# Kernel tuning notes

Measured on AMD Instinct MI355X. Metric: run time of the kernel, lower is better.

The kernel has to match this reference:

```python
import jax, jax.numpy as jnp
import numpy as np

B, T, E, H = 4, 2048, 4096, 128

def setup_inputs() -> dict:
    key = jax.random.key(0)
    ks = jax.random.split(key, 5)
    x = jax.random.normal(ks[0], (B, T, E), dtype=jnp.float32)
    pos_emb = jax.random.normal(ks[1], (B, T, E), dtype=jnp.float32)
    # torch nn.Linear(E, H, bias=False) weights have shape [H, E]
    scale = 1.0 / np.sqrt(E)
    Wq = jax.random.normal(ks[2], (H, E), dtype=jnp.float32) * scale
    Wk = jax.random.normal(ks[3], (H, E), dtype=jnp.float32) * scale
    Wv = jax.random.normal(ks[4], (H, E), dtype=jnp.float32) * scale
    return {"x": x, "pos_emb": pos_emb, "Wq": Wq, "Wk": Wk, "Wv": Wv}

def reference(x, pos_emb, Wq, Wk, Wv):
    Bd, Td, Ed = x.shape
    q = jnp.einsum('bte,he->bth', x, Wq)        # [B,T,H]
    k = jnp.einsum('bte,he->bth', pos_emb, Wk)  # [B,T,H] (key is computed from pos_emb, per source)
    v = jnp.einsum('bte,he->bth', x, Wv)        # [B,T,H]
    # NOTE: source scales by full model dim E**-0.5, not head_size**-0.5
    scores = jnp.einsum('bqh,bkh->bqk', q, k) * (Ed ** -0.5)  # [B,T,T]
    causal = jnp.tril(jnp.ones((Td, Td), dtype=bool))
    scores = jnp.where(causal[None, :, :], scores, -jnp.inf)
    attn = jax.nn.softmax(scores, axis=-1)
    out = jnp.einsum('bqk,bkh->bqh', attn, v)   # [B,T,H]
    return out
```

## Files before the change

### kernel.cpp

```cpp
#include <hip/hip_runtime.h>

#define BB 4
#define TT 2048
#define EE 4096
#define HH 128
#define MM (BB*TT)
#define SCALE 0.015625f

typedef short short8 __attribute__((ext_vector_type(8)));
typedef float f32x4 __attribute__((ext_vector_type(4)));
typedef unsigned short ushort_t;

__device__ __forceinline__ unsigned short f2bf(float x) {
    unsigned int u = __float_as_uint(x);
    u = (u + 0x7fffu + ((u >> 16) & 1u)) >> 16;
    return (unsigned short)u;
}

__global__ __launch_bounds__(256) void wconv(
    const float* __restrict__ Wq, const float* __restrict__ Wk,
    const float* __restrict__ Wv, ushort_t* __restrict__ Wb)
{
    const int gid = blockIdx.x * 256 + threadIdx.x;
    const int which = gid >> 16;
    const int rem = gid & 65535;
    const float* W = (which == 0) ? Wq : (which == 1) ? Wk : Wv;
    const float sc = (which == 0) ? SCALE : 1.0f;
    const float4 f0 = *(const float4*)(W + (size_t)rem * 8);
    const float4 f1 = *(const float4*)(W + (size_t)rem * 8 + 4);
    short8 pk;
    pk[0] = (short)f2bf(f0.x * sc); pk[1] = (short)f2bf(f0.y * sc);
    pk[2] = (short)f2bf(f0.z * sc); pk[3] = (short)f2bf(f0.w * sc);
    pk[4] = (short)f2bf(f1.x * sc); pk[5] = (short)f2bf(f1.y * sc);
    pk[6] = (short)f2bf(f1.z * sc); pk[7] = (short)f2bf(f1.w * sc);
    *(short8*)(Wb + (size_t)which * 524288 + (size_t)rem * 8) = pk;
}

#define ASTR 72

__global__ __launch_bounds__(256) void proj_mfma(
    const float* __restrict__ x, const float* __restrict__ pe,
    const ushort_t* __restrict__ Wb,
    ushort_t* __restrict__ qo, ushort_t* __restrict__ ko_,
    ushort_t* __restrict__ vto)
{
    const int widx = blockIdx.y >> 1;
    const int half = blockIdx.y & 1;
    const float* in = (widx == 1) ? pe : x;
    const ushort_t* W = Wb + (size_t)widx * 524288 + (size_t)half * 64 * EE;

    const int rb   = blockIdx.x * 32;
    const int tid  = threadIdx.x;
    const int lane = tid & 63, wave = tid >> 6;
    const int wr   = wave & 1, wc = wave >> 1;

    __shared__ __align__(16) ushort_t As[32 * ASTR];
    __shared__ __align__(16) ushort_t Bs[64 * ASTR];

    f32x4 acc[2];
    acc[0] = (f32x4){0.f,0.f,0.f,0.f};
    acc[1] = (f32x4){0.f,0.f,0.f,0.f};

    const int fr = lane & 15, quad = lane >> 4, ko = quad * 8;

    const int arow = tid >> 3, aoff = (tid & 7) * 8;
    const float* aptr = in + (size_t)(rb + arow) * EE + aoff;
    const int wrow0 = tid >> 3,        woff0 = (tid & 7) * 8;
    const int wrow1 = wrow0 + 32,      woff1 = woff0;

    float4 pa0 = *(const float4*)(aptr);
    float4 pa1 = *(const float4*)(aptr + 4);
    short8 pw0 = *(const short8*)(W + (size_t)wrow0 * EE + woff0);
    short8 pw1 = *(const short8*)(W + (size_t)wrow1 * EE + woff1);

    for (int k0 = 0; k0 < EE; k0 += 64) {
        {
            short8 a;
            a[0] = (short)f2bf(pa0.x); a[1] = (short)f2bf(pa0.y);
            a[2] = (short)f2bf(pa0.z); a[3] = (short)f2bf(pa0.w);
            a[4] = (short)f2bf(pa1.x); a[5] = (short)f2bf(pa1.y);
            a[6] = (short)f2bf(pa1.z); a[7] = (short)f2bf(pa1.w);
            *(short8*)&As[arow * ASTR + aoff] = a;
            *(short8*)&Bs[wrow0 * ASTR + woff0] = pw0;
            *(short8*)&Bs[wrow1 * ASTR + woff1] = pw1;
        }
        __syncthreads();

        if (k0 + 64 < EE) {
            pa0 = *(const float4*)(aptr + k0 + 64);
            pa1 = *(const float4*)(aptr + k0 + 68);
            pw0 = *(const short8*)(W + (size_t)wrow0 * EE + k0 + 64 + woff0);
            pw1 = *(const short8*)(W + (size_t)wrow1 * EE + k0 + 64 + woff1);
        }

        #pragma unroll
        for (int kk = 0; kk < 64; kk += 32) {
            const short8 af = *(short8*)&As[(wr * 16 + fr) * ASTR + kk + ko];
            #pragma unroll
            for (int t = 0; t < 2; t++) {
                const short8 bf_ = *(short8*)&Bs[(wc * 32 + t * 16 + fr) * ASTR + kk + ko];
                acc[t] = __builtin_amdgcn_mfma_f32_16x16x32_bf16(af, bf_, acc[t], 0, 0, 0);
            }
        }
        __syncthreads();
    }

    const int crow = quad * 4;
    if (widx < 2) {
        ushort_t* out = (widx == 0) ? qo : ko_;
        #pragma unroll
        for (int t = 0; t < 2; t++)
            #pragma unroll
            for (int r = 0; r < 4; r++)
                out[(size_t)(rb + wr * 16 + crow + r) * HH
                    + half * 64 + wc * 32 + t * 16 + fr] = f2bf(acc[t][r]);
    } else {
        ushort_t* T = Bs;
        #pragma unroll
        for (int t = 0; t < 2; t++)
            #pragma unroll
            for (int r = 0; r < 4; r++)
                T[(wc * 32 + t * 16 + fr) * 40 + wr * 16 + crow + r] = f2bf(acc[t][r]);
        __syncthreads();
        const int h64 = tid >> 2, m0 = (tid & 3) * 8;
        const short8 val = *(short8*)&T[h64 * 40 + m0];
        *(short8*)(vto + (size_t)(half * 64 + h64) * MM + rb + m0) = val;
    }
}

__global__ __launch_bounds__(256) void attn_mfma(
    const ushort_t* __restrict__ qb, const ushort_t* __restrict__ kbf,
    const ushort_t* __restrict__ vtb,
    float* __restrict__ OP, float* __restrict__ LP)
{
    const int b = blockIdx.z;
    const int s = blockIdx.y;
    const int t = 63 - (int)blockIdx.x;
    const int tid  = threadIdx.x;
    const int lane = tid & 63, wave = tid >> 6;
    const int fr = lane & 15, quad = lane >> 4, ko = quad * 8;

    const int q0 = t * 32;
    const int C  = (t + 2) >> 1;
    const int cs = (C + 1) >> 1;
    const int c0 = s ? cs : 0;
    const int c1 = s ? C  : cs;

    __shared__ __align__(16) ushort_t Qs[32 * 136];
    __shared__ __align__(16) ushort_t Ks[64 * 136];
    __shared__ __align__(16) ushort_t Vt[128 * 72];
    __shared__ __align__(16) ushort_t Ps[32 * 72];
    __shared__ float lred[2][32];

    for (int f = tid; f < 512; f += 256) {
        const int row = f >> 4, sg = f & 15;
        *(short8*)&Qs[row * 136 + sg * 8] =
            *(const short8*)(qb + (size_t)(b * TT + q0 + row) * HH + sg * 8);
    }

    const int rhS = (wave & 1) * 16, cqS = (wave >> 1) * 32;
    const int rhO = (wave & 1) * 16, chO = (wave >> 1) * 64;

    f32x4 oacc[4];
    #pragma unroll
    for (int i = 0; i < 4; i++) oacc[i] = (f32x4){0.f,0.f,0.f,0.f};
    float lacc[4] = {0.f, 0.f, 0.f, 0.f};

    for (int c = c0; c < c1; c++) {
        const int kb_ = c * 64;
        for (int f = tid; f < 1024; f += 256) {
            const int row = f >> 4, sg = f & 15;
            *(short8*)&Ks[row * 136 + sg * 8] =
                *(const short8*)(kbf + (size_t)(b * TT + kb_ + row) * HH + sg * 8);
        }
        for (int f = tid; f < 1024; f += 256) {
            const int h = f >> 3, sg = f & 7;
            *(short8*)&Vt[h * 72 + sg * 8] =
                *(const short8*)(vtb + (size_t)h * MM + b * TT + kb_ + sg * 8);
        }
        __syncthreads();

        f32x4 sacc[2];
        sacc[0] = (f32x4){0.f,0.f,0.f,0.f};
        sacc[1] = (f32x4){0.f,0.f,0.f,0.f};
        #pragma unroll
        for (int kk = 0; kk < 128; kk += 32) {
            const short8 af = *(short8*)&Qs[(rhS + fr) * 136 + kk + ko];
            const short8 b0 = *(short8*)&Ks[(cqS + fr) * 136 + kk + ko];
            const short8 b1 = *(short8*)&Ks[(cqS + 16 + fr) * 136 + kk + ko];
            sacc[0] = __builtin_amdgcn_mfma_f32_16x16x32_bf16(af, b0, sacc[0], 0, 0, 0);
            sacc[1] = __builtin_amdgcn_mfma_f32_16x16x32_bf16(af, b1, sacc[1], 0, 0, 0);
        }

        #pragma unroll
        for (int tl = 0; tl < 2; tl++)
            #pragma unroll
            for (int r = 0; r < 4; r++) {
                const int row = rhS + quad * 4 + r;
                const int col = cqS + tl * 16 + fr;
                const float p = ((kb_ + col) <= (q0 + row)) ? __expf(sacc[tl][r]) : 0.f;
                lacc[r] += p;
                Ps[row * 72 + col] = f2bf(p);
            }
        __syncthreads();

        #pragma unroll
        for (int ks = 0; ks < 64; ks += 32) {
            const short8 af = *(short8*)&Ps[(rhO + fr) * 72 + ks + ko];
            #pragma unroll
            for (int tl = 0; tl < 4; tl++) {
                const short8 bf_ = *(short8*)&Vt[(chO + tl * 16 + fr) * 72 + ks + ko];
                oacc[tl] = __builtin_amdgcn_mfma_f32_16x16x32_bf16(af, bf_, oacc[tl], 0, 0, 0);
            }
        }
        __syncthreads();
    }

    #pragma unroll
    for (int r = 0; r < 4; r++) {
        float v = lacc[r];
        #pragma unroll
        for (int m = 1; m < 16; m <<= 1) v += __shfl_xor(v, m);
        lacc[r] = v;
    }
    if (fr == 0) {
        #pragma unroll
        for (int r = 0; r < 4; r++)
            lred[wave >> 1][rhS + quad * 4 + r] = lacc[r];
    }
    __syncthreads();
    const int pbase = ((b * 64 + t) * 2 + s);
    if (tid < 32) LP[(size_t)pbase * 32 + tid] = lred[0][tid] + lred[1][tid];

    #pragma unroll
    for (int tl = 0; tl < 4; tl++)
        #pragma unroll
        for (int r = 0; r < 4; r++) {
            const int row = rhO + quad * 4 + r;
            const int col = chO + tl * 16 + fr;
            OP[(size_t)pbase * 4096 + row * 128 + col] = oacc[tl][r];
        }
}

__global__ __launch_bounds__(256) void combine(
    const float* __restrict__ OP, const float* __restrict__ LP,
    float* __restrict__ out)
{
    const int gid = blockIdx.x * 256 + threadIdx.x;
    const int b = gid >> 16;
    const int rem = gid & 65535;
    const int qrow = rem >> 5, h4 = rem & 31;
    const int t = qrow >> 5, r = qrow & 31;
    const int base = (b * 64 + t) * 2;
    const float l = LP[(size_t)base * 32 + r] + LP[(size_t)(base + 1) * 32 + r];
    const float inv = 1.f / l;
    const float4 a = ((const float4*)OP)[(size_t)base * 1024 + r * 32 + h4];
    const float4 c = ((const float4*)OP)[(size_t)(base + 1) * 1024 + r * 32 + h4];
    float4 res;
    res.x = (a.x + c.x) * inv; res.y = (a.y + c.y) * inv;
    res.z = (a.z + c.z) * inv; res.w = (a.w + c.w) * inv;
    ((float4*)out)[gid] = res;
}

extern "C" void kernel_launch(void* const* d_in, const int* in_sizes, int n_in,
                              void* d_out, int out_size, void* d_ws, size_t ws_size,
                              hipStream_t stream) {
    const float* x  = (const float*)d_in[0];
    const float* pe = (const float*)d_in[1];
    const float* Wq = (const float*)d_in[2];
    const float* Wk = (const float*)d_in[3];
    const float* Wv = (const float*)d_in[4];
    float* out = (float*)d_out;

    ushort_t* qb  = (ushort_t*)d_ws;
    ushort_t* kbf = qb  + (size_t)MM * HH;
    ushort_t* vtb = kbf + (size_t)MM * HH;
    ushort_t* Wb  = vtb + (size_t)MM * HH;
    float* OP = (float*)(Wb + (size_t)3 * 128 * 4096);
    float* LP = OP + (size_t)512 * 4096;

    wconv    <<<768, 256, 0, stream>>>(Wq, Wk, Wv, Wb);
    proj_mfma<<<dim3(256, 6), 256, 0, stream>>>(x, pe, Wb, qb, kbf, vtb);
    attn_mfma<<<dim3(64, 2, BB), 256, 0, stream>>>(qb, kbf, vtb, OP, LP);
    combine  <<<1024, 256, 0, stream>>>(OP, LP, out);
}
```

Baseline: 396.0 us.

## Widen projection tile to full head dim with register-resident weight fragments and double buffering

The projection kernel now computes all 128 output columns per block instead of splitting into two halves, so each fp32 input row tile is read and converted to bf16 once rather than twice. Weight fragments are loaded straight from global memory into registers instead of being staged through shared memory. The A tile is double-buffered in LDS with a 128-wide k step, which needs one barrier per step instead of two. In exchange there are half as many blocks (768), more register pressure from 16 prefetched weight fragments and four accumulators, and the non-coalesced per-lane weight loads rely on cache hits.

```diff
diff --git a/kernel.cpp b/kernel.cpp
--- a/kernel.cpp
+++ b/kernel.cpp
@@ -36,7 +36,44 @@
     *(short8*)(Wb + (size_t)which * 524288 + (size_t)rem * 8) = pk;
 }
 
-#define ASTR 72
+#define PSTR 136
+
+#define PACK8(S0, S1, A0, A1, A2, A3) \
+    S0[0]=(short)f2bf(A0.x); S0[1]=(short)f2bf(A0.y); S0[2]=(short)f2bf(A0.z); S0[3]=(short)f2bf(A0.w); \
+    S0[4]=(short)f2bf(A1.x); S0[5]=(short)f2bf(A1.y); S0[6]=(short)f2bf(A1.z); S0[7]=(short)f2bf(A1.w); \
+    S1[0]=(short)f2bf(A2.x); S1[1]=(short)f2bf(A2.y); S1[2]=(short)f2bf(A2.z); S1[3]=(short)f2bf(A2.w); \
+    S1[4]=(short)f2bf(A3.x); S1[5]=(short)f2bf(A3.y); S1[6]=(short)f2bf(A3.z); S1[7]=(short)f2bf(A3.w);
+
+#define PROJ_STEP(KB, BUF, PBC, PBN) do { \
+    const bool more_ = (KB) + 128 < EE; \
+    float4 na0, na1, na2, na3; \
+    if (more_) { \
+        const float* ap_ = aptr + (KB) + 128; \
+        na0 = *(const float4*)ap_;        na1 = *(const float4*)(ap_ + 4); \
+        na2 = *(const float4*)(ap_ + 8);  na3 = *(const float4*)(ap_ + 12); \
+        _Pragma("unroll") \
+        for (int kk = 0; kk < 4; kk++) { \
+            PBN[kk]     = *(const short8*)(wp0 + (KB) + 128 + kk * 32); \
+            PBN[4 + kk] = *(const short8*)(wp1 + (KB) + 128 + kk * 32); \
+        } \
+    } \
+    _Pragma("unroll") \
+    for (int kk = 0; kk < 4; kk++) { \
+        const short8 a0_ = *(const short8*)&As[BUF][fr * PSTR + kk * 32 + ko]; \
+        const short8 a1_ = *(const short8*)&As[BUF][(16 + fr) * PSTR + kk * 32 + ko]; \
+        acc[0][0] = __builtin_amdgcn_mfma_f32_16x16x32_bf16(a0_, PBC[kk],     acc[0][0], 0, 0, 0); \
+        acc[0][1] = __builtin_amdgcn_mfma_f32_16x16x32_bf16(a0_, PBC[4 + kk], acc[0][1], 0, 0, 0); \
+        acc[1][0] = __builtin_amdgcn_mfma_f32_16x16x32_bf16(a1_, PBC[kk],     acc[1][0], 0, 0, 0); \
+        acc[1][1] = __builtin_amdgcn_mfma_f32_16x16x32_bf16(a1_, PBC[4 + kk], acc[1][1], 0, 0, 0); \
+    } \
+    if (more_) { \
+        short8 s0_, s1_; \
+        PACK8(s0_, s1_, na0, na1, na2, na3) \
+        *(short8*)&As[(BUF) ^ 1][arow * PSTR + acol]     = s0_; \
+        *(short8*)&As[(BUF) ^ 1][arow * PSTR + acol + 8] = s1_; \
+        __syncthreads(); \
+    } \
+} while (0)
 
 __global__ __launch_bounds__(256) void proj_mfma(
     const float* __restrict__ x, const float* __restrict__ pe,
@@ -44,87 +81,81 @@
     ushort_t* __restrict__ qo, ushort_t* __restrict__ ko_,
     ushort_t* __restrict__ vto)
 {
-    const int widx = blockIdx.y >> 1;
-    const int half = blockIdx.y & 1;
+    const int widx = blockIdx.y;
     const float* in = (widx == 1) ? pe : x;
-    const ushort_t* W = Wb + (size_t)widx * 524288 + (size_t)half * 64 * EE;
+    const ushort_t* W = Wb + (size_t)widx * 524288;
 
     const int rb   = blockIdx.x * 32;
     const int tid  = threadIdx.x;
     const int lane = tid & 63, wave = tid >> 6;
-    const int wr   = wave & 1, wc = wave >> 1;
-
-    __shared__ __align__(16) ushort_t As[32 * ASTR];
-    __shared__ __align__(16) ushort_t Bs[64 * ASTR];
-
-    f32x4 acc[2];
-    acc[0] = (f32x4){0.f,0.f,0.f,0.f};
-    acc[1] = (f32x4){0.f,0.f,0.f,0.f};
-
     const int fr = lane & 15, quad = lane >> 4, ko = quad * 8;
 
-    const int arow = tid >> 3, aoff = (tid & 7) * 8;
-    const float* aptr = in + (size_t)(rb + arow) * EE + aoff;
-    const int wrow0 = tid >> 3,        woff0 = (tid & 7) * 8;
-    const int wrow1 = wrow0 + 32,      woff1 = woff0;
-
-    float4 pa0 = *(const float4*)(aptr);
-    float4 pa1 = *(const float4*)(aptr + 4);
-    short8 pw0 = *(const short8*)(W + (size_t)wrow0 * EE + woff0);
-    short8 pw1 = *(const short8*)(W + (size_t)wrow1 * EE + woff1);
-
-    for (int k0 = 0; k0 < EE; k0 += 64) {
-        {
-            short8 a;
-            a[0] = (short)f2bf(pa0.x); a[1] = (short)f2bf(pa0.y);
-            a[2] = (short)f2bf(pa0.z); a[3] = (short)f2bf(pa0.w);
-            a[4] = (short)f2bf(pa1.x); a[5] = (short)f2bf(pa1.y);
-            a[6] = (short)f2bf(pa1.z); a[7] = (short)f2bf(pa1.w);
-            *(short8*)&As[arow * ASTR + aoff] = a;
-            *(short8*)&Bs[wrow0 * ASTR + woff0] = pw0;
-            *(short8*)&Bs[wrow1 * ASTR + woff1] = pw1;
-        }
-        __syncthreads();
-
-        if (k0 + 64 < EE) {
-            pa0 = *(const float4*)(aptr + k0 + 64);
-            pa1 = *(const float4*)(aptr + k0 + 68);
-            pw0 = *(const short8*)(W + (size_t)wrow0 * EE + k0 + 64 + woff0);
-            pw1 = *(const short8*)(W + (size_t)wrow1 * EE + k0 + 64 + woff1);
-        }
-
-        #pragma unroll
-        for (int kk = 0; kk < 64; kk += 32) {
-            const short8 af = *(short8*)&As[(wr * 16 + fr) * ASTR + kk + ko];
-            #pragma unroll
-            for (int t = 0; t < 2; t++) {
-                const short8 bf_ = *(short8*)&Bs[(wc * 32 + t * 16 + fr) * ASTR + kk + ko];
-                acc[t] = __builtin_amdgcn_mfma_f32_16x16x32_bf16(af, bf_, acc[t], 0, 0, 0);
-            }
-        }
-        __syncthreads();
+    __shared__ __align__(16) ushort_t As[2][32 * PSTR];
+
+    f32x4 acc[2][2];
+    acc[0][0] = (f32x4){0.f,0.f,0.f,0.f};
+    acc[0][1] = (f32x4){0.f,0.f,0.f,0.f};
+    acc[1][0] = (f32x4){0.f,0.f,0.f,0.f};
+    acc[1][1] = (f32x4){0.f,0.f,0.f,0.f};
+
+    const int arow = tid >> 3, acol = (tid & 7) * 16;
+    const float* aptr = in + (size_t)(rb + arow) * EE + acol;
+
+    const ushort_t* wp0 = W + (size_t)(wave * 32 + fr) * EE + ko;
+    const ushort_t* wp1 = W + (size_t)(wave * 32 + 16 + fr) * EE + ko;
+
+    short8 pbA[8], pbB[8];
+
+    {
+        float4 a0 = *(const float4*)(aptr);
+        float4 a1 = *(const float4*)(aptr + 4);
+        float4 a2 = *(const float4*)(aptr + 8);
+        float4 a3 = *(const float4*)(aptr + 12);
+        #pragma unroll
+        for (int kk = 0; kk < 4; kk++) {
+            pbA[kk]     = *(const short8*)(wp0 + kk * 32);
+            pbA[4 + kk] = *(const short8*)(wp1 + kk * 32);
+        }
+        short8 s0, s1;
+        PACK8(s0, s1, a0, a1, a2, a3)
+        *(short8*)&As[0][arow * PSTR + acol]     = s0;
+        *(short8*)&As[0][arow * PSTR + acol + 8] = s1;
+        __syncthreads();
+    }
+
+    for (int k0 = 0; k0 < EE; k0 += 256) {
+        PROJ_STEP(k0,       0, pbA, pbB);
+        PROJ_STEP(k0 + 128, 1, pbB, pbA);
     }
 
     const int crow = quad * 4;
     if (widx < 2) {
         ushort_t* out = (widx == 0) ? qo : ko_;
         #pragma unroll
-        for (int t = 0; t < 2; t++)
+        for (int rg = 0; rg < 2; rg++)
             #pragma unroll
-            for (int r = 0; r < 4; r++)
-                out[(size_t)(rb + wr * 16 + crow + r) * HH
-                    + half * 64 + wc * 32 + t * 16 + fr] = f2bf(acc[t][r]);
+            for (int cg = 0; cg < 2; cg++)
+                #pragma unroll
+                for (int r = 0; r < 4; r++)
+                    out[(size_t)(rb + rg * 16 + crow + r) * HH
+                        + wave * 32 + cg * 16 + fr] = f2bf(acc[rg][cg][r]);
     } else {
-        ushort_t* T = Bs;
-        #pragma unroll
-        for (int t = 0; t < 2; t++)
+        __syncthreads();
+        ushort_t* T = (ushort_t*)As;
+        #pragma unroll
+        for (int rg = 0; rg < 2; rg++)
             #pragma unroll
-            for (int r = 0; r < 4; r++)
-                T[(wc * 32 + t * 16 + fr) * 40 + wr * 16 + crow + r] = f2bf(acc[t][r]);
-        __syncthreads();
-        const int h64 = tid >> 2, m0 = (tid & 3) * 8;
-        const short8 val = *(short8*)&T[h64 * 40 + m0];
-        *(short8*)(vto + (size_t)(half * 64 + h64) * MM + rb + m0) = val;
+            for (int cg = 0; cg < 2; cg++)
+                #pragma unroll
+                for (int r = 0; r < 4; r++)
+                    T[(wave * 32 + cg * 16 + fr) * 40 + rg * 16 + crow + r]
+                        = f2bf(acc[rg][cg][r]);
+        __syncthreads();
+        const int col = tid >> 1, m0 = (tid & 1) * 16;
+        const short8 v0 = *(short8*)&T[col * 40 + m0];
+        const short8 v1 = *(short8*)&T[col * 40 + m0 + 8];
+        *(short8*)(vto + (size_t)col * MM + rb + m0)     = v0;
+        *(short8*)(vto + (size_t)col * MM + rb + m0 + 8) = v1;
     }
 }
 
@@ -280,7 +311,7 @@
     float* LP = OP + (size_t)512 * 4096;
 
     wconv    <<<768, 256, 0, stream>>>(Wq, Wk, Wv, Wb);
-    proj_mfma<<<dim3(256, 6), 256, 0, stream>>>(x, pe, Wb, qb, kbf, vtb);
+    proj_mfma<<<dim3(256, 3), 256, 0, stream>>>(x, pe, Wb, qb, kbf, vtb);
     attn_mfma<<<dim3(64, 2, BB), 256, 0, stream>>>(qb, kbf, vtb, OP, LP);
     combine  <<<1024, 256, 0, stream>>>(OP, LP, out);
 }
```

Result: faster. 386.6 us (-2.4%).

## Retile projection GEMM to 128x128 tiles with split-K and async LDS loads

Applied to the files above, without the earlier changes.

The projection GEMM now gives each block a 128-row tile covering all 128 head columns, with a 4x4 MFMA accumulator per wave. Each block handles a quarter of the K dimension, and a new combine kernel sums the fp32 partials and writes bf16 q/k and transposed v. Weight tiles are staged into double-buffered LDS with global_load_lds, and the fp32 input is prefetched in registers. The intent is to stop re-reading x twice per weight half and to raise MFMA reuse. In exchange there is an extra kernel and fp32 partial traffic through a workspace that is shared with the attention partial buffers.

```diff
diff --git a/kernel.cpp b/kernel.cpp
--- a/kernel.cpp
+++ b/kernel.cpp
@@ -10,11 +10,18 @@
 typedef short short8 __attribute__((ext_vector_type(8)));
 typedef float f32x4 __attribute__((ext_vector_type(4)));
 typedef unsigned short ushort_t;
+typedef unsigned int u32;
 
 __device__ __forceinline__ unsigned short f2bf(float x) {
     unsigned int u = __float_as_uint(x);
     u = (u + 0x7fffu + ((u >> 16) & 1u)) >> 16;
     return (unsigned short)u;
+}
+
+__device__ __forceinline__ void gl_lds16(const ushort_t* g, ushort_t* l) {
+    __builtin_amdgcn_global_load_lds(
+        (const __attribute__((address_space(1))) u32*)(g),
+        (__attribute__((address_space(3))) u32*)(l), 16, 0, 0);
 }
 
 __global__ __launch_bounds__(256) void wconv(
@@ -36,95 +43,175 @@
     *(short8*)(Wb + (size_t)which * 524288 + (size_t)rem * 8) = pk;
 }
 
-#define ASTR 72
+#define KSPLIT 4
+#define KSPAN  1024
+#define KSTEP  64
+#define NSTEPS 16
+#define ASTRIDE 72
 
 __global__ __launch_bounds__(256) void proj_mfma(
     const float* __restrict__ x, const float* __restrict__ pe,
-    const ushort_t* __restrict__ Wb,
+    const ushort_t* __restrict__ Wb, float* __restrict__ Pp)
+{
+    const int mb   = blockIdx.x;
+    const int widx = blockIdx.y;
+    const int sp   = blockIdx.z;
+    const float* in = (widx == 1) ? pe : x;
+    const ushort_t* W = Wb + (size_t)widx * (128 * EE);
+
+    const int rb    = mb * 128;
+    const int kbase = sp * KSPAN;
+
+    const int tid  = threadIdx.x;
+    const int lane = tid & 63, wave = tid >> 6;
+    const int wr = wave & 1, wc = wave >> 1;
+    const int fr = lane & 15, quad = lane >> 4, ko = quad * 8;
+
+    __shared__ __align__(16) ushort_t Asl[128 * ASTRIDE];
+    __shared__ __align__(16) ushort_t Bsl[2][128 * KSTEP];
+
+    f32x4 acc[4][4];
+    #pragma unroll
+    for (int m = 0; m < 4; m++)
+        #pragma unroll
+        for (int n = 0; n < 4; n++) acc[m][n] = (f32x4){0.f,0.f,0.f,0.f};
+
+    const int arow = tid >> 1;
+    const int acol = (tid & 1) * 32;
+    const float* aptr = in + (size_t)(rb + arow) * EE + kbase + acol;
+
+    const ushort_t* bsrc = W + (size_t)(tid >> 3) * EE + kbase + (tid & 7) * 8;
+    const int bdst = tid * 8;
+
+    float4 ar[8];
+
+#define LOAD_A(KOFS) do { \
+    const float* p_ = aptr + (KOFS); \
+    _Pragma("unroll") \
+    for (int j = 0; j < 8; j++) ar[j] = *(const float4*)(p_ + j * 4); \
+} while (0)
+
+#define STAGE_B(KOFS, BUF) do { \
+    _Pragma("unroll") \
+    for (int j = 0; j < 4; j++) \
+        gl_lds16(bsrc + (KOFS) + (size_t)j * 32 * EE, \
+                 &Bsl[BUF][bdst + j * 2048]); \
+} while (0)
+
+#define WRITE_A() do { \
+    _Pragma("unroll") \
+    for (int j = 0; j < 4; j++) { \
+        short8 s_; \
+        const float4 a0_ = ar[2*j], a1_ = ar[2*j+1]; \
+        s_[0]=(short)f2bf(a0_.x); s_[1]=(short)f2bf(a0_.y); \
+        s_[2]=(short)f2bf(a0_.z); s_[3]=(short)f2bf(a0_.w); \
+        s_[4]=(short)f2bf(a1_.x); s_[5]=(short)f2bf(a1_.y); \
+        s_[6]=(short)f2bf(a1_.z); s_[7]=(short)f2bf(a1_.w); \
+        *(short8*)&Asl[arow * ASTRIDE + acol + j * 8] = s_; \
+    } \
+} while (0)
+
+    LOAD_A(0);
+    STAGE_B(0, 0);
+    WRITE_A();
+    __syncthreads();
+
+    for (int s = 0; s < NSTEPS; s++) {
+        const int buf = s & 1;
+        const bool more = (s + 1 < NSTEPS);
+        if (more) {
+            LOAD_A((s + 1) * KSTEP);
+            STAGE_B((s + 1) * KSTEP, buf ^ 1);
+        }
+        #pragma unroll
+        for (int h = 0; h < 2; h++) {
+            short8 af[4], bf_[4];
+            #pragma unroll
+            for (int m = 0; m < 4; m++)
+                af[m] = *(short8*)&Asl[(wr*64 + m*16 + fr) * ASTRIDE + h*32 + ko];
+            #pragma unroll
+            for (int n = 0; n < 4; n++)
+                bf_[n] = *(short8*)&Bsl[buf][(wc*64 + n*16 + fr) * KSTEP + h*32 + ko];
+            #pragma unroll
+            for (int m = 0; m < 4; m++)
+                #pragma unroll
+                for (int n = 0; n < 4; n++)
+                    acc[m][n] = __builtin_amdgcn_mfma_f32_16x16x32_bf16(
+                        af[m], bf_[n], acc[m][n], 0, 0, 0);
+        }
+        __syncthreads();
+        if (more) {
+            WRITE_A();
+            __syncthreads();
+        }
+    }
+
+    float* P = Pp + ((size_t)(widx * KSPLIT + sp) * MM + rb) * HH;
+    #pragma unroll
+    for (int m = 0; m < 4; m++)
+        #pragma unroll
+        for (int n = 0; n < 4; n++)
+            #pragma unroll
+            for (int r = 0; r < 4; r++)
+                P[(size_t)(wr*64 + m*16 + quad*4 + r) * HH
+                  + wc*64 + n*16 + fr] = acc[m][n][r];
+
+#undef LOAD_A
+#undef STAGE_B
+#undef WRITE_A
+}
+
+__global__ __launch_bounds__(256) void projcomb(
+    const float* __restrict__ Pp,
     ushort_t* __restrict__ qo, ushort_t* __restrict__ ko_,
     ushort_t* __restrict__ vto)
 {
-    const int widx = blockIdx.y >> 1;
-    const int half = blockIdx.y & 1;
-    const float* in = (widx == 1) ? pe : x;
-    const ushort_t* W = Wb + (size_t)widx * 524288 + (size_t)half * 64 * EE;
-
-    const int rb   = blockIdx.x * 32;
+    const int mb   = blockIdx.x;
+    const int widx = blockIdx.y;
     const int tid  = threadIdx.x;
-    const int lane = tid & 63, wave = tid >> 6;
-    const int wr   = wave & 1, wc = wave >> 1;
-
-    __shared__ __align__(16) ushort_t As[32 * ASTR];
-    __shared__ __align__(16) ushort_t Bs[64 * ASTR];
-
-    f32x4 acc[2];
-    acc[0] = (f32x4){0.f,0.f,0.f,0.f};
-    acc[1] = (f32x4){0.f,0.f,0.f,0.f};
-
-    const int fr = lane & 15, quad = lane >> 4, ko = quad * 8;
-
-    const int arow = tid >> 3, aoff = (tid & 7) * 8;
-    const float* aptr = in + (size_t)(rb + arow) * EE + aoff;
-    const int wrow0 = tid >> 3,        woff0 = (tid & 7) * 8;
-    const int wrow1 = wrow0 + 32,      woff1 = woff0;
-
-    float4 pa0 = *(const float4*)(aptr);
-    float4 pa1 = *(const float4*)(aptr + 4);
-    short8 pw0 = *(const short8*)(W + (size_t)wrow0 * EE + woff0);
-    short8 pw1 = *(const short8*)(W + (size_t)wrow1 * EE + woff1);
-
-    for (int k0 = 0; k0 < EE; k0 += 64) {
-        {
-            short8 a;
-            a[0] = (short)f2bf(pa0.x); a[1] = (short)f2bf(pa0.y);
-            a[2] = (short)f2bf(pa0.z); a[3] = (short)f2bf(pa0.w);
-            a[4] = (short)f2bf(pa1.x); a[5] = (short)f2bf(pa1.y);
-            a[6] = (short)f2bf(pa1.z); a[7] = (short)f2bf(pa1.w);
-            *(short8*)&As[arow * ASTR + aoff] = a;
-            *(short8*)&Bs[wrow0 * ASTR + woff0] = pw0;
-            *(short8*)&Bs[wrow1 * ASTR + woff1] = pw1;
-        }
-        __syncthreads();
-
-        if (k0 + 64 < EE) {
-            pa0 = *(const float4*)(aptr + k0 + 64);
-            pa1 = *(const float4*)(aptr + k0 + 68);
-            pw0 = *(const short8*)(W + (size_t)wrow0 * EE + k0 + 64 + woff0);
-            pw1 = *(const short8*)(W + (size_t)wrow1 * EE + k0 + 64 + woff1);
-        }
-
-        #pragma unroll
-        for (int kk = 0; kk < 64; kk += 32) {
-            const short8 af = *(short8*)&As[(wr * 16 + fr) * ASTR + kk + ko];
-            #pragma unroll
-            for (int t = 0; t < 2; t++) {
-                const short8 bf_ = *(short8*)&Bs[(wc * 32 + t * 16 + fr) * ASTR + kk + ko];
-                acc[t] = __builtin_amdgcn_mfma_f32_16x16x32_bf16(af, bf_, acc[t], 0, 0, 0);
-            }
-        }
-        __syncthreads();
-    }
-
-    const int crow = quad * 4;
+    const int m0 = mb * 64;
+    const int r_ = tid >> 2;
+    const int h0 = (tid & 3) * 32;
+
+    __shared__ ushort_t T[128 * 72];
+
+    const float* base = Pp + ((size_t)widx * KSPLIT * MM + m0 + r_) * HH + h0;
+    float accv[32];
+    #pragma unroll
+    for (int j = 0; j < 8; j++) {
+        float4 a = *(const float4*)(base + j * 4);
+        accv[4*j+0] = a.x; accv[4*j+1] = a.y; accv[4*j+2] = a.z; accv[4*j+3] = a.w;
+    }
+    #pragma unroll
+    for (int s = 1; s < KSPLIT; s++) {
+        const float* bs = base + (size_t)s * MM * HH;
+        #pragma unroll
+        for (int j = 0; j < 8; j++) {
+            float4 a = *(const float4*)(bs + j * 4);
+            accv[4*j+0] += a.x; accv[4*j+1] += a.y;
+            accv[4*j+2] += a.z; accv[4*j+3] += a.w;
+        }
+    }
+
     if (widx < 2) {
         ushort_t* out = (widx == 0) ? qo : ko_;
         #pragma unroll
-        for (int t = 0; t < 2; t++)
-            #pragma unroll
-            for (int r = 0; r < 4; r++)
-                out[(size_t)(rb + wr * 16 + crow + r) * HH
-                    + half * 64 + wc * 32 + t * 16 + fr] = f2bf(acc[t][r]);
+        for (int j = 0; j < 4; j++) {
+            short8 s_;
+            #pragma unroll
+            for (int e = 0; e < 8; e++) s_[e] = (short)f2bf(accv[j*8 + e]);
+            *(short8*)&out[(size_t)(m0 + r_) * HH + h0 + j * 8] = s_;
+        }
     } else {
-        ushort_t* T = Bs;
-        #pragma unroll
-        for (int t = 0; t < 2; t++)
-            #pragma unroll
-            for (int r = 0; r < 4; r++)
-                T[(wc * 32 + t * 16 + fr) * 40 + wr * 16 + crow + r] = f2bf(acc[t][r]);
-        __syncthreads();
-        const int h64 = tid >> 2, m0 = (tid & 3) * 8;
-        const short8 val = *(short8*)&T[h64 * 40 + m0];
-        *(short8*)(vto + (size_t)(half * 64 + h64) * MM + rb + m0) = val;
+        #pragma unroll
+        for (int e = 0; e < 32; e++)
+            T[(h0 + e) * 72 + r_] = f2bf(accv[e]);
+        __syncthreads();
+        const int h = tid >> 1, ms = (tid & 1) * 32;
+        #pragma unroll
+        for (int j = 0; j < 4; j++)
+            *(short8*)&vto[(size_t)h * MM + m0 + ms + j * 8]
+                = *(short8*)&T[h * 72 + ms + j * 8];
     }
 }
 
@@ -276,11 +363,13 @@
     ushort_t* kbf = qb  + (size_t)MM * HH;
     ushort_t* vtb = kbf + (size_t)MM * HH;
     ushort_t* Wb  = vtb + (size_t)MM * HH;
-    float* OP = (float*)(Wb + (size_t)3 * 128 * 4096);
+    float* Pp = (float*)(Wb + (size_t)3 * 128 * 4096);
+    float* OP = Pp;
     float* LP = OP + (size_t)512 * 4096;
 
     wconv    <<<768, 256, 0, stream>>>(Wq, Wk, Wv, Wb);
-    proj_mfma<<<dim3(256, 6), 256, 0, stream>>>(x, pe, Wb, qb, kbf, vtb);
+    proj_mfma<<<dim3(64, 3, KSPLIT), 256, 0, stream>>>(x, pe, Wb, Pp);
+    projcomb <<<dim3(128, 3), 256, 0, stream>>>(Pp, qb, kbf, vtb);
     attn_mfma<<<dim3(64, 2, BB), 256, 0, stream>>>(qb, kbf, vtb, OP, LP);
     combine  <<<1024, 256, 0, stream>>>(OP, LP, out);
 }
```

Result: no change. 402.8 us (+1.7%).
